# Optimization experiments

Measured on AMD Instinct MI355X. Metric: run time of the kernel, lower is better.

Reference implementation:

```python
import jax, jax.numpy as jnp
import numpy as np

DT = 1.0
V_LAMBDA = 1e-4
V_RIDGE = 1e-4


def third_order_D(Np):
    # [Np-3, Np] banded third-difference operator
    M = Np - 3
    r = jnp.arange(M)
    D = jnp.zeros((M, Np), dtype=jnp.float32)
    D = D.at[r, r].set(-1.0).at[r, r + 1].set(3.0).at[r, r + 2].set(-3.0).at[r, r + 3].set(1.0)
    return D


def setup_inputs() -> dict:
    key = jax.random.key(0)
    k1, k2, k3 = jax.random.split(key, 3)
    B, N = 8192, 64
    dxy = jax.random.normal(k1, (B, N, 2), dtype=jnp.float32)
    theta = jax.random.normal(k2, (B, N + 1), dtype=jnp.float32)
    v0 = jax.random.normal(k3, (B,), dtype=jnp.float32)
    return {"dxy": dxy, "theta": theta, "v0": v0}


def reference(dxy, theta, v0):
    B, N, _ = dxy.shape  # theta: [B, N+1]
    g = (2.0 / DT) * dxy                     # [B, N, 2]
    b = g.reshape(B, 2 * N)                  # interleaved (x, y) per step
    cos_t = jnp.cos(theta)
    sin_t = jnp.sin(theta)

    # Assemble banded data matrix A: [B, 2N, N+1]
    rows = jnp.arange(N)
    A = jnp.zeros((B, 2 * N, N + 1), dtype=dxy.dtype)
    A = A.at[:, 2 * rows, rows].set(cos_t[:, :-1])
    A = A.at[:, 2 * rows, rows + 1].set(cos_t[:, 1:])
    A = A.at[:, 2 * rows + 1, rows].set(sin_t[:, :-1])
    A = A.at[:, 2 * rows + 1, rows + 1].set(sin_t[:, 1:])
    # data weights w = 1 -> Aw == A

    ATA = jnp.einsum('bij,bik->bjk', A, A)           # [B, N+1, N+1]
    rhs = jnp.einsum('bij,bi->bj', A[:, :, 1:], b)   # [B, N]
    rhs = rhs - ATA[:, 1:, 0] * v0[:, None]

    # Smoothness prior: third-order difference, lam3 = v_lambda / dt^6
    D3 = third_order_D(N + 1)
    DTD = (V_LAMBDA / DT ** 6) * (D3.T @ D3)         # [N+1, N+1], shared across batch
    rhs = rhs - DTD[1:, 0] * v0[:, None]

    lhs = ATA[:, 1:, 1:] + DTD[1:, 1:] + V_RIDGE * jnp.eye(N, dtype=dxy.dtype)
    L = jnp.linalg.cholesky(lhs)
    y = jax.scipy.linalg.cho_solve((L, True), rhs[..., None])[..., 0]  # [B, N]
    return jnp.concatenate([v0[:, None], y], axis=-1)                  # [B, N+1]
```

## Files before the change

### kernel.cpp

```cpp
#include <hip/hip_runtime.h>
#include <math.h>

#define LAM3  1e-4f
#define RIDGE 1e-4f
#define NN    64
#define NP    65

__device__ __forceinline__ float d3_diag(int f) {
    if (f == 0 || f == 64) return 1.f;
    if (f == 1 || f == 63) return 10.f;
    if (f == 2 || f == 62) return 19.f;
    return 20.f;
}
__device__ __forceinline__ float d3_off1(int f) {
    if (f == 1 || f == 64) return -3.f;
    if (f == 2 || f == 63) return -12.f;
    return -15.f;
}
__device__ __forceinline__ float d3_off2(int f) {
    if (f == 2 || f == 64) return 3.f;
    return 6.f;
}

__global__ __launch_bounds__(64, 1) void alpamayo_banded_solve(
    const float* __restrict__ dxy,
    const float* __restrict__ theta,
    const float* __restrict__ v0,
    float* __restrict__ out,
    int B)
{
    __shared__ float4 Lrec[NN][64];

    const int tid = threadIdx.x;
    const int b = blockIdx.x * 64 + tid;
    if (b >= B) return;

    const float* th = theta + (long)b * NP;
    const float4* dx4 = (const float4*)(dxy + (long)b * (2 * NN));
    const float v0b = v0[b];

    float thr[NP];
    #pragma unroll
    for (int f = 0; f < NP; ++f) thr[f] = th[f];
    float dxf[2 * NN];
    #pragma unroll
    for (int j = 0; j < 32; ++j) {
        const float4 q = dx4[j];
        dxf[4 * j + 0] = q.x; dxf[4 * j + 1] = q.y;
        dxf[4 * j + 2] = q.z; dxf[4 * j + 3] = q.w;
    }

    float c[NP], s[NP];
    #pragma unroll
    for (int f = 0; f < NP; ++f) __sincosf(thr[f], &s[f], &c[f]);

    float rhs[NN], e[NN];
    #pragma unroll
    for (int i = 0; i < NN; ++i) {
        const int f = i + 1;
        const float bx = dxf[2 * f - 2] + (f < NN ? dxf[2 * f] : 0.f);
        const float by = dxf[2 * f - 1] + (f < NN ? dxf[2 * f + 1] : 0.f);
        rhs[i] = 2.f * (c[f] * bx + s[f] * by);
        e[i] = c[i] * c[f] + s[i] * s[f];
    }
    rhs[0] -= (e[0] + LAM3 * -3.f) * v0b;
    rhs[1] -= (LAM3 *  3.f) * v0b;
    rhs[2] -= (LAM3 * -1.f) * v0b;

    float z[NN];
    float p1L1 = 0.f, p1L2 = 0.f, p2L1 = 0.f;
    float rd1 = 0.f, rd2 = 0.f, rd3 = 0.f;
    float z1 = 0.f, z2 = 0.f, z3 = 0.f;

    #pragma unroll
    for (int i = 0; i < NN; ++i) {
        const int f = i + 1;
        const float a0 = (f == NN ? 1.f : 2.f) + LAM3 * d3_diag(f) + RIDGE;
        const float a1 = e[i] + LAM3 * d3_off1(f);
        const float a2 = LAM3 * d3_off2(f);
        const float a3 = LAM3 * -1.f;

        const float Li3 = a3 * rd3;
        const float Li2 = (a2 - Li3 * p2L1) * rd2;
        const float Li1 = (a1 - Li3 * p1L2 - Li2 * p1L1) * rd1;
        const float dg  = a0 - Li3 * Li3 - Li2 * Li2 - Li1 * Li1;
        const float rd0 = __builtin_amdgcn_rsqf(dg);

        const float zi = (rhs[i] - Li3 * z3 - Li2 * z2 - Li1 * z1) * rd0;

        Lrec[i][tid] = make_float4(Li1, Li2, Li3, rd0);
        z[i] = zi;

        p2L1 = p1L1; p1L1 = Li1; p1L2 = Li2;
        rd3 = rd2; rd2 = rd1; rd1 = rd0;
        z3 = z2; z2 = z1; z1 = zi;
    }

    float r1L1 = 0.f, r1L2 = 0.f, r1L3 = 0.f;
    float r2L2 = 0.f, r2L3 = 0.f;
    float r3L3 = 0.f;
    float y1 = 0.f, y2 = 0.f, y3 = 0.f;

    float* outp = out + (long)b * NP;

    #pragma unroll
    for (int i = NN - 1; i >= 0; --i) {
        const float4 rec = Lrec[i][tid];
        const float yi = (z[i] - r1L1 * y1 - r2L2 * y2 - r3L3 * y3) * rec.w;
        outp[1 + i] = yi;
        r3L3 = r2L3; r2L3 = r1L3; r2L2 = r1L2;
        r1L1 = rec.x; r1L2 = rec.y; r1L3 = rec.z;
        y3 = y2; y2 = y1; y1 = yi;
    }
    outp[0] = v0b;
}

extern "C" void kernel_launch(void* const* d_in, const int* in_sizes, int n_in,
                              void* d_out, int out_size, void* d_ws, size_t ws_size,
                              hipStream_t stream) {
    const float* dxy   = (const float*)d_in[0];
    const float* theta = (const float*)d_in[1];
    const float* v0    = (const float*)d_in[2];
    float* out = (float*)d_out;
    const int B = in_sizes[2];
    const int blocks = (B + 63) / 64;
    alpamayo_banded_solve<<<blocks, 64, 0, stream>>>(dxy, theta, v0, out, B);
}
```

Measured before the change: 64.18 us.

## Stage inputs and outputs through shared memory with coalesced loads and 32 rows per block

Each block now covers 32 batch rows instead of 64, and loads theta and dxy into padded shared memory cooperatively with coalesced global reads. Results are staged back through shared memory and written out coalesced. Before, each thread read and wrote its own strided row. The aim is better memory coalescing and twice as many blocks to fill the GPU. The cost is that half the threads in each 64-thread block sit idle during the solve, plus extra barriers and more shared memory.

Result: slower. 94.48 us (+47.2%).

```diff
diff --git a/kernel.cpp b/kernel.cpp
--- a/kernel.cpp
+++ b/kernel.cpp
@@ -5,6 +5,13 @@
 #define RIDGE 1e-4f
 #define NN    64
 #define NP    65
+#define ROWS  32
+
+#define LREC_WORDS (NN * ROWS * 4)
+#define TH_OFF     LREC_WORDS
+#define DXY_OFF    (TH_OFF + ROWS * NP)
+#define OUT_OFF    DXY_OFF
+#define SMEM_WORDS (DXY_OFF + ROWS * 129)
 
 __device__ __forceinline__ float d3_diag(int f) {
     if (f == 0 || f == 64) return 1.f;
@@ -29,90 +36,123 @@
     float* __restrict__ out,
     int B)
 {
-    __shared__ float4 Lrec[NN][64];
+    __shared__ __align__(16) float smem[SMEM_WORDS];
 
-    const int tid = threadIdx.x;
-    const int b = blockIdx.x * 64 + tid;
-    if (b >= B) return;
+    const int tid  = threadIdx.x;
+    const int base = blockIdx.x * ROWS;
+    const int rows = (B - base < ROWS) ? (B - base) : ROWS;
 
-    const float* th = theta + (long)b * NP;
-    const float4* dx4 = (const float4*)(dxy + (long)b * (2 * NN));
-    const float v0b = v0[b];
+    {
+        const float* thg = theta + (long)base * NP;
+        const int nth = rows * NP;
+        #pragma unroll
+        for (int w = 0; w < (ROWS * NP + 63) / 64; ++w) {
+            const int idx = w * 64 + tid;
+            if (idx < nth) smem[TH_OFF + idx] = thg[idx];
+        }
+        const float* dg = dxy + (long)base * (2 * NN);
+        const int ndx = rows * 2 * NN;
+        #pragma unroll
+        for (int w = 0; w < (ROWS * 2 * NN) / 64; ++w) {
+            const int idx = w * 64 + tid;
+            if (idx < ndx) {
+                const int r = idx >> 7, c = idx & 127;
+                smem[DXY_OFF + r * 129 + c] = dg[idx];
+            }
+        }
+    }
+    __syncthreads();
 
-    float thr[NP];
-    #pragma unroll
-    for (int f = 0; f < NP; ++f) thr[f] = th[f];
-    float dxf[2 * NN];
-    #pragma unroll
-    for (int j = 0; j < 32; ++j) {
-        const float4 q = dx4[j];
-        dxf[4 * j + 0] = q.x; dxf[4 * j + 1] = q.y;
-        dxf[4 * j + 2] = q.z; dxf[4 * j + 3] = q.w;
+    const bool active = tid < rows;
+    float z[NN];
+    float v0b = 0.f;
+
+    if (active) {
+        v0b = v0[base + tid];
+        const float* th = smem + TH_OFF  + tid * NP;
+        const float* dx = smem + DXY_OFF + tid * 129;
+
+        float rhs[NN], e[NN];
+        float cp, sp;
+        __sincosf(th[0], &sp, &cp);
+        float xc = dx[0], yc = dx[1];
+        #pragma unroll
+        for (int f = 1; f <= NN; ++f) {
+            float cf, sf;
+            __sincosf(th[f], &sf, &cf);
+            e[f - 1] = cf * cp + sf * sp;
+            const float xn = (f < NN) ? dx[2 * f]     : 0.f;
+            const float yn = (f < NN) ? dx[2 * f + 1] : 0.f;
+            rhs[f - 1] = 2.f * (cf * (xc + xn) + sf * (yc + yn));
+            cp = cf; sp = sf; xc = xn; yc = yn;
+        }
+        rhs[0] -= (e[0] + LAM3 * -3.f) * v0b;
+        rhs[1] -= (LAM3 *  3.f) * v0b;
+        rhs[2] -= (LAM3 * -1.f) * v0b;
+
+        float4* Lr = (float4*)smem;
+        float p1L1 = 0.f, p1L2 = 0.f, p2L1 = 0.f;
+        float rd1 = 0.f, rd2 = 0.f, rd3 = 0.f;
+        float z1 = 0.f, z2 = 0.f, z3 = 0.f;
+
+        #pragma unroll
+        for (int i = 0; i < NN; ++i) {
+            const int f = i + 1;
+            const float a0 = (f == NN ? 1.f : 2.f) + LAM3 * d3_diag(f) + RIDGE;
+            const float a1 = e[i] + LAM3 * d3_off1(f);
+            const float a2 = LAM3 * d3_off2(f);
+            const float a3 = LAM3 * -1.f;
+
+            const float Li3 = a3 * rd3;
+            const float Li2 = (a2 - Li3 * p2L1) * rd2;
+            const float Li1 = (a1 - Li3 * p1L2 - Li2 * p1L1) * rd1;
+            const float dg  = a0 - Li3 * Li3 - Li2 * Li2 - Li1 * Li1;
+            const float rd0 = __builtin_amdgcn_rsqf(dg);
+
+            const float zi = (rhs[i] - Li3 * z3 - Li2 * z2 - Li1 * z1) * rd0;
+
+            Lr[i * ROWS + tid] = make_float4(Li1, Li2, Li3, rd0);
+            z[i] = zi;
+
+            p2L1 = p1L1; p1L1 = Li1; p1L2 = Li2;
+            rd3 = rd2; rd2 = rd1; rd1 = rd0;
+            z3 = z2; z2 = z1; z1 = zi;
+        }
+
+        float r1L1 = 0.f, r1L2 = 0.f, r1L3 = 0.f;
+        float r2L2 = 0.f, r2L3 = 0.f;
+        float r3L3 = 0.f;
+        float y1 = 0.f, y2 = 0.f, y3 = 0.f;
+
+        #pragma unroll
+        for (int i = NN - 1; i >= 0; --i) {
+            const float4 rec = Lr[i * ROWS + tid];
+            const float yi = (z[i] - r1L1 * y1 - r2L2 * y2 - r3L3 * y3) * rec.w;
+            z[i] = yi;
+            r3L3 = r2L3; r2L3 = r1L3; r2L2 = r1L2;
+            r1L1 = rec.x; r1L2 = rec.y; r1L3 = rec.z;
+            y3 = y2; y2 = y1; y1 = yi;
+        }
     }
 
-    float c[NP], s[NP];
-    #pragma unroll
-    for (int f = 0; f < NP; ++f) __sincosf(thr[f], &s[f], &c[f]);
+    __syncthreads();
+    if (active) {
+        float* os = smem + OUT_OFF + tid * NP;
+        os[0] = v0b;
+        #pragma unroll
+        for (int i = 0; i < NN; ++i) os[1 + i] = z[i];
+    }
+    __syncthreads();
 
-    float rhs[NN], e[NN];
-    #pragma unroll
-    for (int i = 0; i < NN; ++i) {
-        const int f = i + 1;
-        const float bx = dxf[2 * f - 2] + (f < NN ? dxf[2 * f] : 0.f);
-        const float by = dxf[2 * f - 1] + (f < NN ? dxf[2 * f + 1] : 0.f);
-        rhs[i] = 2.f * (c[f] * bx + s[f] * by);
-        e[i] = c[i] * c[f] + s[i] * s[f];
+    {
+        float* og = out + (long)base * NP;
+        const int nout = rows * NP;
+        #pragma unroll
+        for (int w = 0; w < (ROWS * NP + 63) / 64; ++w) {
+            const int idx = w * 64 + tid;
+            if (idx < nout) og[idx] = smem[OUT_OFF + idx];
+        }
     }
-    rhs[0] -= (e[0] + LAM3 * -3.f) * v0b;
-    rhs[1] -= (LAM3 *  3.f) * v0b;
-    rhs[2] -= (LAM3 * -1.f) * v0b;
-
-    float z[NN];
-    float p1L1 = 0.f, p1L2 = 0.f, p2L1 = 0.f;
-    float rd1 = 0.f, rd2 = 0.f, rd3 = 0.f;
-    float z1 = 0.f, z2 = 0.f, z3 = 0.f;
-
-    #pragma unroll
-    for (int i = 0; i < NN; ++i) {
-        const int f = i + 1;
-        const float a0 = (f == NN ? 1.f : 2.f) + LAM3 * d3_diag(f) + RIDGE;
-        const float a1 = e[i] + LAM3 * d3_off1(f);
-        const float a2 = LAM3 * d3_off2(f);
-        const float a3 = LAM3 * -1.f;
-
-        const float Li3 = a3 * rd3;
-        const float Li2 = (a2 - Li3 * p2L1) * rd2;
-        const float Li1 = (a1 - Li3 * p1L2 - Li2 * p1L1) * rd1;
-        const float dg  = a0 - Li3 * Li3 - Li2 * Li2 - Li1 * Li1;
-        const float rd0 = __builtin_amdgcn_rsqf(dg);
-
-        const float zi = (rhs[i] - Li3 * z3 - Li2 * z2 - Li1 * z1) * rd0;
-
-        Lrec[i][tid] = make_float4(Li1, Li2, Li3, rd0);
-        z[i] = zi;
-
-        p2L1 = p1L1; p1L1 = Li1; p1L2 = Li2;
-        rd3 = rd2; rd2 = rd1; rd1 = rd0;
-        z3 = z2; z2 = z1; z1 = zi;
-    }
-
-    float r1L1 = 0.f, r1L2 = 0.f, r1L3 = 0.f;
-    float r2L2 = 0.f, r2L3 = 0.f;
-    float r3L3 = 0.f;
-    float y1 = 0.f, y2 = 0.f, y3 = 0.f;
-
-    float* outp = out + (long)b * NP;
-
-    #pragma unroll
-    for (int i = NN - 1; i >= 0; --i) {
-        const float4 rec = Lrec[i][tid];
-        const float yi = (z[i] - r1L1 * y1 - r2L2 * y2 - r3L3 * y3) * rec.w;
-        outp[1 + i] = yi;
-        r3L3 = r2L3; r2L3 = r1L3; r2L2 = r1L2;
-        r1L1 = rec.x; r1L2 = rec.y; r1L3 = rec.z;
-        y3 = y2; y2 = y1; y1 = yi;
-    }
-    outp[0] = v0b;
 }
 
 extern "C" void kernel_launch(void* const* d_in, const int* in_sizes, int n_in,
@@ -123,6 +163,6 @@
     const float* v0    = (const float*)d_in[2];
     float* out = (float*)d_out;
     const int B = in_sizes[2];
-    const int blocks = (B + 63) / 64;
+    const int blocks = (B + ROWS - 1) / ROWS;
     alpamayo_banded_solve<<<blocks, 64, 0, stream>>>(dxy, theta, v0, out, B);
 }
```

## Stage outputs in shared memory for coalesced stores and keep L factors in registers

Applied to the files above, without the earlier changes.

Each block now solves 32 batch rows using half of its 64 lanes, keeping the Cholesky factors in registers instead of shared memory. Results are staged in shared memory and written back by all 64 threads as contiguous, coalesced stores, replacing the strided per-thread stores of before. The sincos loop is also fused with the e/rhs assembly. The cost is that half the lanes sit idle during the solve, register pressure rises, and twice as many blocks are launched.

Result: slower. 66.41 us (+3.5%).

```diff
diff --git a/kernel.cpp b/kernel.cpp
--- a/kernel.cpp
+++ b/kernel.cpp
@@ -5,6 +5,7 @@
 #define RIDGE 1e-4f
 #define NN    64
 #define NP    65
+#define ROWS  32
 
 __device__ __forceinline__ float d3_diag(int f) {
     if (f == 0 || f == 64) return 1.f;
@@ -29,90 +30,113 @@
     float* __restrict__ out,
     int B)
 {
-    __shared__ float4 Lrec[NN][64];
+    __shared__ float outs[ROWS * NP + 32];
 
-    const int tid = threadIdx.x;
-    const int b = blockIdx.x * 64 + tid;
-    if (b >= B) return;
+    const int tid  = threadIdx.x;
+    const int base = blockIdx.x * ROWS;
 
-    const float* th = theta + (long)b * NP;
-    const float4* dx4 = (const float4*)(dxy + (long)b * (2 * NN));
-    const float v0b = v0[b];
+    if (tid < ROWS) {
+        int b = base + tid;
+        if (b >= B) b = B - 1;
 
-    float thr[NP];
-    #pragma unroll
-    for (int f = 0; f < NP; ++f) thr[f] = th[f];
-    float dxf[2 * NN];
-    #pragma unroll
-    for (int j = 0; j < 32; ++j) {
-        const float4 q = dx4[j];
-        dxf[4 * j + 0] = q.x; dxf[4 * j + 1] = q.y;
-        dxf[4 * j + 2] = q.z; dxf[4 * j + 3] = q.w;
+        const float*  th  = theta + (long)b * NP;
+        const float4* dx4 = (const float4*)(dxy + (long)b * (2 * NN));
+        const float   v0b = v0[b];
+
+        float dxf[2 * NN];
+        #pragma unroll
+        for (int j = 0; j < 32; ++j) {
+            const float4 q = dx4[j];
+            dxf[4 * j + 0] = q.x; dxf[4 * j + 1] = q.y;
+            dxf[4 * j + 2] = q.z; dxf[4 * j + 3] = q.w;
+        }
+        float thr[NP];
+        #pragma unroll
+        for (int f = 0; f < NP; ++f) thr[f] = th[f];
+
+        float e[NN], rhs[NN];
+        {
+            float cp, sp;
+            __sincosf(thr[0], &sp, &cp);
+            #pragma unroll
+            for (int f = 1; f <= NN; ++f) {
+                float cf, sf;
+                __sincosf(thr[f], &sf, &cf);
+                e[f - 1] = cf * cp + sf * sp;
+                const float xn = (f < NN) ? dxf[2 * f]     : 0.f;
+                const float yn = (f < NN) ? dxf[2 * f + 1] : 0.f;
+                rhs[f - 1] = 2.f * (cf * (dxf[2 * f - 2] + xn) + sf * (dxf[2 * f - 1] + yn));
+                cp = cf; sp = sf;
+            }
+        }
+        rhs[0] -= (e[0] + LAM3 * -3.f) * v0b;
+        rhs[1] -= (LAM3 *  3.f) * v0b;
+        rhs[2] -= (LAM3 * -1.f) * v0b;
+
+        float  z[NN];
+        float4 Lr[NN];
+        float p1L1 = 0.f, p1L2 = 0.f, p2L1 = 0.f;
+        float rd1 = 0.f, rd2 = 0.f, rd3 = 0.f;
+        float z1 = 0.f, z2 = 0.f, z3 = 0.f;
+
+        #pragma unroll
+        for (int i = 0; i < NN; ++i) {
+            const int f = i + 1;
+            const float a0 = (f == NN ? 1.f : 2.f) + LAM3 * d3_diag(f) + RIDGE;
+            const float a1 = e[i] + LAM3 * d3_off1(f);
+            const float a2 = LAM3 * d3_off2(f);
+            const float a3 = LAM3 * -1.f;
+
+            const float Li3 = a3 * rd3;
+            const float Li2 = (a2 - Li3 * p2L1) * rd2;
+            const float Li1 = (a1 - Li3 * p1L2 - Li2 * p1L1) * rd1;
+            const float dg  = a0 - Li3 * Li3 - Li2 * Li2 - Li1 * Li1;
+            const float rd0 = __builtin_amdgcn_rsqf(dg);
+
+            const float zi = (rhs[i] - Li3 * z3 - Li2 * z2 - Li1 * z1) * rd0;
+
+            Lr[i] = make_float4(Li1, Li2, Li3, rd0);
+            z[i] = zi;
+
+            p2L1 = p1L1; p1L1 = Li1; p1L2 = Li2;
+            rd3 = rd2; rd2 = rd1; rd1 = rd0;
+            z3 = z2; z2 = z1; z1 = zi;
+        }
+
+        float r1L1 = 0.f, r1L2 = 0.f, r1L3 = 0.f;
+        float r2L2 = 0.f, r2L3 = 0.f;
+        float r3L3 = 0.f;
+        float y1 = 0.f, y2 = 0.f, y3 = 0.f;
+
+        #pragma unroll
+        for (int i = NN - 1; i >= 0; --i) {
+            const float4 rec = Lr[i];
+            const float yi = (z[i] - r1L1 * y1 - r2L2 * y2 - r3L3 * y3) * rec.w;
+            z[i] = yi;
+            r3L3 = r2L3; r2L3 = r1L3; r2L2 = r1L2;
+            r1L1 = rec.x; r1L2 = rec.y; r1L3 = rec.z;
+            y3 = y2; y2 = y1; y1 = yi;
+        }
+
+        float* os = outs + tid * NP;
+        os[0] = v0b;
+        #pragma unroll
+        for (int i = 0; i < NN; ++i) os[1 + i] = z[i];
     }
 
-    float c[NP], s[NP];
-    #pragma unroll
-    for (int f = 0; f < NP; ++f) __sincosf(thr[f], &s[f], &c[f]);
+    __syncthreads();
 
-    float rhs[NN], e[NN];
-    #pragma unroll
-    for (int i = 0; i < NN; ++i) {
-        const int f = i + 1;
-        const float bx = dxf[2 * f - 2] + (f < NN ? dxf[2 * f] : 0.f);
-        const float by = dxf[2 * f - 1] + (f < NN ? dxf[2 * f + 1] : 0.f);
-        rhs[i] = 2.f * (c[f] * bx + s[f] * by);
-        e[i] = c[i] * c[f] + s[i] * s[f];
+    {
+        int nv = B - base;
+        if (nv > ROWS) nv = ROWS;
+        const int nvalid = nv * NP;
+        float* og = out + (long)base * NP;
+        #pragma unroll
+        for (int w = 0; w < (ROWS * NP + 63) / 64; ++w) {
+            const int idx = w * 64 + tid;
+            if (idx < nvalid) og[idx] = outs[idx];
+        }
     }
-    rhs[0] -= (e[0] + LAM3 * -3.f) * v0b;
-    rhs[1] -= (LAM3 *  3.f) * v0b;
-    rhs[2] -= (LAM3 * -1.f) * v0b;
-
-    float z[NN];
-    float p1L1 = 0.f, p1L2 = 0.f, p2L1 = 0.f;
-    float rd1 = 0.f, rd2 = 0.f, rd3 = 0.f;
-    float z1 = 0.f, z2 = 0.f, z3 = 0.f;
-
-    #pragma unroll
-    for (int i = 0; i < NN; ++i) {
-        const int f = i + 1;
-        const float a0 = (f == NN ? 1.f : 2.f) + LAM3 * d3_diag(f) + RIDGE;
-        const float a1 = e[i] + LAM3 * d3_off1(f);
-        const float a2 = LAM3 * d3_off2(f);
-        const float a3 = LAM3 * -1.f;
-
-        const float Li3 = a3 * rd3;
-        const float Li2 = (a2 - Li3 * p2L1) * rd2;
-        const float Li1 = (a1 - Li3 * p1L2 - Li2 * p1L1) * rd1;
-        const float dg  = a0 - Li3 * Li3 - Li2 * Li2 - Li1 * Li1;
-        const float rd0 = __builtin_amdgcn_rsqf(dg);
-
-        const float zi = (rhs[i] - Li3 * z3 - Li2 * z2 - Li1 * z1) * rd0;
-
-        Lrec[i][tid] = make_float4(Li1, Li2, Li3, rd0);
-        z[i] = zi;
-
-        p2L1 = p1L1; p1L1 = Li1; p1L2 = Li2;
-        rd3 = rd2; rd2 = rd1; rd1 = rd0;
-        z3 = z2; z2 = z1; z1 = zi;
-    }
-
-    float r1L1 = 0.f, r1L2 = 0.f, r1L3 = 0.f;
-    float r2L2 = 0.f, r2L3 = 0.f;
-    float r3L3 = 0.f;
-    float y1 = 0.f, y2 = 0.f, y3 = 0.f;
-
-    float* outp = out + (long)b * NP;
-
-    #pragma unroll
-    for (int i = NN - 1; i >= 0; --i) {
-        const float4 rec = Lrec[i][tid];
-        const float yi = (z[i] - r1L1 * y1 - r2L2 * y2 - r3L3 * y3) * rec.w;
-        outp[1 + i] = yi;
-        r3L3 = r2L3; r2L3 = r1L3; r2L2 = r1L2;
-        r1L1 = rec.x; r1L2 = rec.y; r1L3 = rec.z;
-        y3 = y2; y2 = y1; y1 = yi;
-    }
-    outp[0] = v0b;
 }
 
 extern "C" void kernel_launch(void* const* d_in, const int* in_sizes, int n_in,
@@ -123,6 +147,6 @@
     const float* v0    = (const float*)d_in[2];
     float* out = (float*)d_out;
     const int B = in_sizes[2];
-    const int blocks = (B + 63) / 64;
+    const int blocks = (B + ROWS - 1) / ROWS;
     alpamayo_banded_solve<<<blocks, 64, 0, stream>>>(dxy, theta, v0, out, B);
 }
```

## Stage rows through LDS with coalesced loads/stores, 32 rows per block

Applied to the files above, without the earlier changes.

Each block now handles 32 batch rows. All 64 lanes cooperatively load theta and dxy into shared memory with coalesced strided accesses, and the output is staged in shared memory and written back coalesced. Sincos and the rhs terms are computed on the fly inside the factorization loop, which replaces the large per-thread register arrays, and only the L1/L2 factors and reciprocal diagonals are stored in shared memory. This targets the uncoalesced per-thread global accesses and high register pressure of the old version. The cost is that only half the lanes do the serial solve, the block needs more shared memory, and two barriers are added.

After: 75.02 us. 16.9% more time.

```diff
diff --git a/kernel.cpp b/kernel.cpp
--- a/kernel.cpp
+++ b/kernel.cpp
@@ -5,6 +5,7 @@
 #define RIDGE 1e-4f
 #define NN    64
 #define NP    65
+#define ROWS  32
 
 __device__ __forceinline__ float d3_diag(int f) {
     if (f == 0 || f == 64) return 1.f;
@@ -29,90 +30,147 @@
     float* __restrict__ out,
     int B)
 {
-    __shared__ float4 Lrec[NN][64];
+    __shared__ float  th_s[NP * ROWS];
+    __shared__ float  dx_s[128 * ROWS];
+    __shared__ float2 L12s[NN * ROWS];
+    __shared__ float  rds [NN * ROWS];
+    __shared__ float  outs[NP * ROWS];
+    __shared__ float4 Atab[NN];
 
-    const int tid = threadIdx.x;
-    const int b = blockIdx.x * 64 + tid;
-    if (b >= B) return;
-
-    const float* th = theta + (long)b * NP;
-    const float4* dx4 = (const float4*)(dxy + (long)b * (2 * NN));
-    const float v0b = v0[b];
-
-    float thr[NP];
-    #pragma unroll
-    for (int f = 0; f < NP; ++f) thr[f] = th[f];
-    float dxf[2 * NN];
-    #pragma unroll
-    for (int j = 0; j < 32; ++j) {
-        const float4 q = dx4[j];
-        dxf[4 * j + 0] = q.x; dxf[4 * j + 1] = q.y;
-        dxf[4 * j + 2] = q.z; dxf[4 * j + 3] = q.w;
+    const int lane = threadIdx.x;
+    long base = (long)blockIdx.x * ROWS;
+    bool fastB = true;
+    if (base + ROWS > B) {
+        base = B - ROWS;
+        if (base < 0) { base = 0; fastB = false; }
     }
 
-    float c[NP], s[NP];
-    #pragma unroll
-    for (int f = 0; f < NP; ++f) __sincosf(thr[f], &s[f], &c[f]);
-
-    float rhs[NN], e[NN];
-    #pragma unroll
-    for (int i = 0; i < NN; ++i) {
-        const int f = i + 1;
-        const float bx = dxf[2 * f - 2] + (f < NN ? dxf[2 * f] : 0.f);
-        const float by = dxf[2 * f - 1] + (f < NN ? dxf[2 * f + 1] : 0.f);
-        rhs[i] = 2.f * (c[f] * bx + s[f] * by);
-        e[i] = c[i] * c[f] + s[i] * s[f];
-    }
-    rhs[0] -= (e[0] + LAM3 * -3.f) * v0b;
-    rhs[1] -= (LAM3 *  3.f) * v0b;
-    rhs[2] -= (LAM3 * -1.f) * v0b;
-
-    float z[NN];
-    float p1L1 = 0.f, p1L2 = 0.f, p2L1 = 0.f;
-    float rd1 = 0.f, rd2 = 0.f, rd3 = 0.f;
-    float z1 = 0.f, z2 = 0.f, z3 = 0.f;
-
-    #pragma unroll
-    for (int i = 0; i < NN; ++i) {
-        const int f = i + 1;
-        const float a0 = (f == NN ? 1.f : 2.f) + LAM3 * d3_diag(f) + RIDGE;
-        const float a1 = e[i] + LAM3 * d3_off1(f);
-        const float a2 = LAM3 * d3_off2(f);
-        const float a3 = LAM3 * -1.f;
-
-        const float Li3 = a3 * rd3;
-        const float Li2 = (a2 - Li3 * p2L1) * rd2;
-        const float Li1 = (a1 - Li3 * p1L2 - Li2 * p1L1) * rd1;
-        const float dg  = a0 - Li3 * Li3 - Li2 * Li2 - Li1 * Li1;
-        const float rd0 = __builtin_amdgcn_rsqf(dg);
-
-        const float zi = (rhs[i] - Li3 * z3 - Li2 * z2 - Li1 * z1) * rd0;
-
-        Lrec[i][tid] = make_float4(Li1, Li2, Li3, rd0);
-        z[i] = zi;
-
-        p2L1 = p1L1; p1L1 = Li1; p1L2 = Li2;
-        rd3 = rd2; rd2 = rd1; rd1 = rd0;
-        z3 = z2; z2 = z1; z1 = zi;
+    if (lane < NN) {
+        const int f = lane + 1;
+        const float a0  = (f == NN ? 1.f : 2.f) + LAM3 * d3_diag(f) + RIDGE;
+        const float a1c = LAM3 * d3_off1(f);
+        const float a2  = LAM3 * d3_off2(f);
+        float cv = 0.f;
+        if (lane == 0) cv = -3.f * LAM3;
+        if (lane == 1) cv =  3.f * LAM3;
+        if (lane == 2) cv = -1.f * LAM3;
+        Atab[lane] = make_float4(a0, a1c, a2, cv);
     }
 
-    float r1L1 = 0.f, r1L2 = 0.f, r1L3 = 0.f;
-    float r2L2 = 0.f, r2L3 = 0.f;
-    float r3L3 = 0.f;
-    float y1 = 0.f, y2 = 0.f, y3 = 0.f;
+    if (fastB) {
+        const int lo = lane & 31, hi = lane >> 5;
+        const float* tg = theta + (base + lo) * NP + hi;
+        #pragma unroll
+        for (int w = 0; w < 32; ++w) th_s[w * 64 + lane] = tg[2 * w];
+        if (lane < 32) th_s[NN * 32 + lane] = theta[(base + lane) * NP + NN];
+        const float* dg_ = dxy + (base + lo) * (2 * NN) + hi;
+        #pragma unroll
+        for (int w = 0; w < 64; ++w) dx_s[w * 64 + lane] = dg_[2 * w];
+    } else {
+        if (lane < B) {
+            for (int f = 0; f < NP; ++f)  th_s[f * 32 + lane] = theta[((long)lane) * NP + f];
+            for (int c = 0; c < 128; ++c) dx_s[c * 32 + lane] = dxy[((long)lane) * (2 * NN) + c];
+        }
+    }
+    long v0i = base + (lane & 31); if (v0i > (long)B - 1) v0i = B - 1;
+    const float v0b = v0[v0i];
 
-    float* outp = out + (long)b * NP;
+    __syncthreads();
 
-    #pragma unroll
-    for (int i = NN - 1; i >= 0; --i) {
-        const float4 rec = Lrec[i][tid];
-        const float yi = (z[i] - r1L1 * y1 - r2L2 * y2 - r3L3 * y3) * rec.w;
-        outp[1 + i] = yi;
-        r3L3 = r2L3; r2L3 = r1L3; r2L2 = r1L2;
-        r1L1 = rec.x; r1L2 = rec.y; r1L3 = rec.z;
-        y3 = y2; y2 = y1; y1 = yi;
+    if (lane < ROWS) {
+        const int l = lane;
+        float cp, sp;
+        __sincosf(th_s[0 * 32 + l], &sp, &cp);
+        float xc = dx_s[0 * 32 + l], yc = dx_s[1 * 32 + l];
+        float thn = th_s[1 * 32 + l];
+        float xn  = dx_s[2 * 32 + l], yn = dx_s[3 * 32 + l];
+
+        float p1L1 = 0.f, p1L2 = 0.f, p2L1 = 0.f;
+        float rd1 = 0.f, rd2 = 0.f, rd3 = 0.f;
+        float z1 = 0.f, z2 = 0.f, z3 = 0.f;
+        float* oz = outs + l * NP;
+        oz[0] = v0b;
+
+        #pragma unroll 4
+        for (int i = 0; i < NN; ++i) {
+            const int f = i + 1;
+            const float thf = thn;
+            const float xf = xn, yf = yn;
+            const int f2 = (f < NN) ? f + 1 : NN;
+            thn = th_s[f2 * 32 + l];
+            const int c2 = (f < NN - 1) ? 2 * f + 2 : 126;
+            xn = dx_s[c2 * 32 + l];
+            yn = dx_s[(c2 + 1) * 32 + l];
+
+            float cf, sf;
+            __sincosf(thf, &sf, &cf);
+            const float e  = cf * cp + sf * sp;
+            const float xs = (f < NN) ? xf : 0.f;
+            const float ys = (f < NN) ? yf : 0.f;
+            const float4 a = Atab[i];
+            float rr = 2.f * (cf * (xc + xs) + sf * (yc + ys));
+            rr -= a.w * v0b;
+            if (i == 0) rr -= e * v0b;
+
+            const float a1  = e + a.y;
+            const float Li3 = (-LAM3) * rd3;
+            const float Li2 = (a.z - Li3 * p2L1) * rd2;
+            const float Li1 = (a1 - Li3 * p1L2 - Li2 * p1L1) * rd1;
+            const float dg  = a.x - Li3 * Li3 - Li2 * Li2 - Li1 * Li1;
+            const float rd0 = __builtin_amdgcn_rsqf(dg);
+            const float zi  = (rr - Li3 * z3 - Li2 * z2 - Li1 * z1) * rd0;
+
+            L12s[i * 32 + l] = make_float2(Li1, Li2);
+            rds [i * 32 + l] = rd0;
+            oz[1 + i] = zi;
+
+            p2L1 = p1L1; p1L1 = Li1; p1L2 = Li2;
+            rd3 = rd2; rd2 = rd1; rd1 = rd0;
+            z3 = z2; z2 = z1; z1 = zi;
+            cp = cf; sp = sf; xc = xs; yc = ys;
+        }
+
+        float r1L1 = 0.f, r1L2 = 0.f, r1L3 = 0.f;
+        float r2L2 = 0.f, r2L3 = 0.f, r3L3 = 0.f;
+        float y1 = 0.f, y2 = 0.f, y3 = 0.f;
+
+        float2 Lc  = L12s[(NN - 1) * 32 + l];
+        float  rdc = rds [(NN - 1) * 32 + l];
+        float  zc  = oz[NN];
+        float  rm3 = rds [(NN - 4) * 32 + l];
+
+        #pragma unroll 4
+        for (int i = NN - 1; i >= 0; --i) {
+            const float L1i = Lc.x, L2i = Lc.y, rdi = rdc, zi = zc, rdm3 = rm3;
+            const int ip  = (i > 0)  ? i - 1 : 0;
+            Lc  = L12s[ip * 32 + l];
+            rdc = rds [ip * 32 + l];
+            zc  = oz[ip + 1];
+            const int im4 = (i >= 4) ? i - 4 : 0;
+            rm3 = rds[im4 * 32 + l];
+
+            const float L3i = (i >= 3) ? (-LAM3) * rdm3 : 0.f;
+            const float yi  = (zi - r1L1 * y1 - r2L2 * y2 - r3L3 * y3) * rdi;
+            oz[1 + i] = yi;
+
+            r3L3 = r2L3; r2L3 = r1L3; r2L2 = r1L2;
+            r1L1 = L1i;  r1L2 = L2i;  r1L3 = L3i;
+            y3 = y2; y2 = y1; y1 = yi;
+        }
     }
-    outp[0] = v0b;
+
+    __syncthreads();
+
+    {
+        long nv = B - base; if (nv > ROWS) nv = ROWS;
+        const int nvalid = (int)nv * NP;
+        float* og = out + base * NP;
+        #pragma unroll
+        for (int w = 0; w < 33; ++w) {
+            const int q = w * 64 + lane;
+            if (q < nvalid) og[q] = outs[q];
+        }
+    }
 }
 
 extern "C" void kernel_launch(void* const* d_in, const int* in_sizes, int n_in,
@@ -123,6 +181,6 @@
     const float* v0    = (const float*)d_in[2];
     float* out = (float*)d_out;
     const int B = in_sizes[2];
-    const int blocks = (B + 63) / 64;
+    const int blocks = (B + ROWS - 1) / ROWS;
     alpamayo_banded_solve<<<blocks, 64, 0, stream>>>(dxy, theta, v0, out, B);
 }
```
